# Optimization experiments

Hardware: AMD Instinct MI355X
Metric: run time of the kernel (lower is better)

The kernel has to match this reference:

```python
import jax, jax.numpy as jnp
import numpy as np

N_NODES = 100000
N_EDGES = 1600000
IN_FEATS, N_HIDDEN, N_CLASSES = 128, 64, 40


def setup_inputs() -> dict:
    key = jax.random.key(0)
    ks = jax.random.split(key, 6)
    h = jax.random.normal(ks[0], (N_NODES, IN_FEATS), dtype=jnp.float32)
    W0 = jax.random.normal(ks[1], (IN_FEATS, N_HIDDEN), dtype=jnp.float32) * (1.0 / np.sqrt(IN_FEATS))
    b0 = jnp.zeros((N_HIDDEN,), dtype=jnp.float32)
    W1 = jax.random.normal(ks[2], (N_HIDDEN, N_HIDDEN), dtype=jnp.float32) * (1.0 / np.sqrt(N_HIDDEN))
    b1 = jnp.zeros((N_HIDDEN,), dtype=jnp.float32)
    W2 = jax.random.normal(ks[3], (N_HIDDEN, N_CLASSES), dtype=jnp.float32) * (1.0 / np.sqrt(N_HIDDEN))
    b2 = jnp.zeros((N_CLASSES,), dtype=jnp.float32)
    src = jax.random.randint(ks[4], (N_EDGES,), 0, N_NODES, dtype=jnp.int32)
    dst = jax.random.randint(ks[5], (N_EDGES,), 0, N_NODES, dtype=jnp.int32)
    return {"h": h, "W0": W0, "b0": b0, "W1": W1, "b1": b1, "W2": W2, "b2": b2, "src": src, "dst": dst}


def _degrees(src, dst):
    ones = jnp.ones(src.shape[0], dtype=jnp.float32)
    out_deg = jax.ops.segment_sum(ones, src, num_segments=N_NODES)
    in_deg = jax.ops.segment_sum(ones, dst, num_segments=N_NODES)
    # DGL clamps degrees to >= 1 (allow_zero_in_degree)
    norm_src = jax.lax.rsqrt(jnp.maximum(out_deg, 1.0))  # [N]
    norm_dst = jax.lax.rsqrt(jnp.maximum(in_deg, 1.0))   # [N]
    return norm_src, norm_dst


def _graph_conv(x, W, b, src, dst, norm_src, norm_dst, act):
    # DGL GraphConv, norm='both': D_in^{-1/2} A^T D_out^{-1/2} (X W) + b
    xw = (x @ W) * norm_src[:, None]               # [N, out]
    agg = jax.ops.segment_sum(xw[src], dst, num_segments=N_NODES)  # gather-scatter over edges
    out = agg * norm_dst[:, None] + b
    return jax.nn.relu(out) if act else out


def reference(h, W0, b0, W1, b1, W2, b2, src, dst):
    norm_src, norm_dst = _degrees(src, dst)
    h = _graph_conv(h, W0, b0, src, dst, norm_src, norm_dst, act=True)
    # dropout layers are identity at inference
    h = _graph_conv(h, W1, b1, src, dst, norm_src, norm_dst, act=True)
    h = _graph_conv(h, W2, b2, src, dst, norm_src, norm_dst, act=False)
    return h
```

## Files before the change

kernel.cpp:

```cpp
#include <hip/hip_runtime.h>
#include <hip/hip_fp16.h>

#define N_NODES 100000
#define N_EDGES 1600000
#define ELL_W 64
#define NCHUNK 64
#define NSEG 4
#define CH (N_EDGES / NCHUNK)
#define SEGN (N_NODES / NSEG)

typedef _Float16 half8 __attribute__((ext_vector_type(8)));
typedef float floatx4 __attribute__((ext_vector_type(4)));


__global__ __launch_bounds__(512) void k_count(const int* __restrict__ src, const int* __restrict__ dst,
                                               unsigned char* __restrict__ cnt_out,
                                               unsigned char* __restrict__ cnt_in) {
    __shared__ unsigned pk[SEGN];
    const int c = blockIdx.x;
    const int lo = blockIdx.y * SEGN;
    for (int i = threadIdx.x; i < SEGN; i += 512) pk[i] = 0;
    __syncthreads();
    const int4* s4 = (const int4*)(src + c * CH);
    const int4* d4 = (const int4*)(dst + c * CH);
    for (int i = threadIdx.x; i < CH / 4; i += 512) {
        int4 s = s4[i], d = d4[i];
        unsigned a;
        a = (unsigned)(s.x - lo); if (a < SEGN) atomicAdd(&pk[a], 0x10000u);
        a = (unsigned)(s.y - lo); if (a < SEGN) atomicAdd(&pk[a], 0x10000u);
        a = (unsigned)(s.z - lo); if (a < SEGN) atomicAdd(&pk[a], 0x10000u);
        a = (unsigned)(s.w - lo); if (a < SEGN) atomicAdd(&pk[a], 0x10000u);
        a = (unsigned)(d.x - lo); if (a < SEGN) atomicAdd(&pk[a], 1u);
        a = (unsigned)(d.y - lo); if (a < SEGN) atomicAdd(&pk[a], 1u);
        a = (unsigned)(d.z - lo); if (a < SEGN) atomicAdd(&pk[a], 1u);
        a = (unsigned)(d.w - lo); if (a < SEGN) atomicAdd(&pk[a], 1u);
    }
    __syncthreads();
    for (int i = threadIdx.x; i < SEGN; i += 512) {
        unsigned v = pk[i];
        cnt_in [c * N_NODES + lo + i] = (unsigned char)(v & 0xFFFF);
        cnt_out[c * N_NODES + lo + i] = (unsigned char)(v >> 16);
    }
}

__global__ __launch_bounds__(256) void k_scan(unsigned char* __restrict__ cnt_in,
                                              const unsigned char* __restrict__ cnt_out,
                                              int* __restrict__ fill, float* __restrict__ norm_src,
                                              float* __restrict__ norm_dst) {
    int d = blockIdx.x * 256 + threadIdx.x;
    if (d >= N_NODES) return;
    int run = 0;
    for (int c = 0; c < NCHUNK; ++c) {
        int v = cnt_in[c * N_NODES + d];
        cnt_in[c * N_NODES + d] = (unsigned char)run;
        run += v;
    }
    int od = 0;
    for (int c = 0; c < NCHUNK; ++c) od += cnt_out[c * N_NODES + d];
    fill[d] = run;
    norm_dst[d] = rsqrtf((float)(run < 1 ? 1 : run));
    norm_src[d] = rsqrtf((float)(od  < 1 ? 1 : od ));
}

__global__ __launch_bounds__(512) void k_scatter(const int* __restrict__ src, const int* __restrict__ dst,
                                                 const unsigned char* __restrict__ bases,
                                                 int* __restrict__ ell) {
    __shared__ unsigned base[SEGN / 2];
    const int c = blockIdx.x;
    const int lo = blockIdx.y * SEGN;
    for (int i = threadIdx.x; i < SEGN / 2; i += 512) {
        unsigned b0 = bases[c * N_NODES + lo + 2 * i];
        unsigned b1 = bases[c * N_NODES + lo + 2 * i + 1];
        base[i] = b0 | (b1 << 16);
    }
    __syncthreads();
    const int4* s4 = (const int4*)(src + c * CH);
    const int4* d4 = (const int4*)(dst + c * CH);
    for (int i = threadIdx.x; i < CH / 4; i += 512) {
        int4 s = s4[i], d = d4[i];
        unsigned r, sh, old; int p;
        r = (unsigned)(d.x - lo); if (r < SEGN) { sh = (r & 1) << 4; old = atomicAdd(&base[r >> 1], 1u << sh); p = (old >> sh) & 0xFFFF; if (p < ELL_W) ell[p * N_NODES + lo + r] = s.x; }
        r = (unsigned)(d.y - lo); if (r < SEGN) { sh = (r & 1) << 4; old = atomicAdd(&base[r >> 1], 1u << sh); p = (old >> sh) & 0xFFFF; if (p < ELL_W) ell[p * N_NODES + lo + r] = s.y; }
        r = (unsigned)(d.z - lo); if (r < SEGN) { sh = (r & 1) << 4; old = atomicAdd(&base[r >> 1], 1u << sh); p = (old >> sh) & 0xFFFF; if (p < ELL_W) ell[p * N_NODES + lo + r] = s.z; }
        r = (unsigned)(d.w - lo); if (r < SEGN) { sh = (r & 1) << 4; old = atomicAdd(&base[r >> 1], 1u << sh); p = (old >> sh) & 0xFFFF; if (p < ELL_W) ell[p * N_NODES + lo + r] = s.w; }
    }
}

__device__ __forceinline__ void acc16B(const float4& v, float* acc) {
    const __half2* hh = (const __half2*)&v;
    #pragma unroll
    for (int t = 0; t < 4; ++t) {
        float2 f = __half22float2(hh[t]);
        acc[2 * t + 0] += f.x;
        acc[2 * t + 1] += f.y;
    }
}

template<int K, int NCOL>
__global__ __launch_bounds__(256) void k_gemm(const float* __restrict__ Xv, const float* __restrict__ W,
                                              const float* __restrict__ norm, __half* __restrict__ Y) {
    constexpr int NT = (NCOL + 15) / 16;
    constexpr int NR = NT * 16;
    __shared__ __align__(16) _Float16 Xh[64][K + 8];
    __shared__ __align__(16) _Float16 Wt[NR][K + 8];
    const int tid = threadIdx.x;
    const int row0 = blockIdx.x * 64;

    for (int idx = tid; idx < K * NCOL; idx += 256) {
        int k = idx / NCOL, c = idx - (idx / NCOL) * NCOL;
        Wt[c][k] = (_Float16)W[idx];
    }
    for (int idx = tid; idx < (NR - NCOL) * K; idx += 256) {
        int c = NCOL + idx / K, k = idx - (idx / K) * K;
        Wt[c][k] = (_Float16)0;
    }

    for (int idx = tid; idx < 64 * (K / 8); idx += 256) {
        int r = idx / (K / 8), kc = idx - (idx / (K / 8)) * (K / 8);
        int gr = row0 + r;
        half8 v = {0, 0, 0, 0, 0, 0, 0, 0};
        if (gr < N_NODES) {
            const float* X = Xv + (long)gr * K + kc * 8;
            float4 u0 = *(const float4*)(X + 0);
            float4 u1 = *(const float4*)(X + 4);
            v.s0 = (_Float16)u0.x; v.s1 = (_Float16)u0.y;
            v.s2 = (_Float16)u0.z; v.s3 = (_Float16)u0.w;
            v.s4 = (_Float16)u1.x; v.s5 = (_Float16)u1.y;
            v.s6 = (_Float16)u1.z; v.s7 = (_Float16)u1.w;
        }
        *(half8*)&Xh[r][kc * 8] = v;
    }
    __syncthreads();

    const int lane = tid & 63;
    const int wave = tid >> 6;
    const int quad = lane >> 4;
    const int l16 = lane & 15;
    const int r0 = wave * 16;

    floatx4 acc[NT] = {};
    #pragma unroll
    for (int k0 = 0; k0 < K; k0 += 32) {
        half8 a = *(const half8*)&Xh[r0 + l16][k0 + quad * 8];
        #pragma unroll
        for (int t = 0; t < NT; ++t) {
            half8 b = *(const half8*)&Wt[t * 16 + l16][k0 + quad * 8];
            acc[t] = __builtin_amdgcn_mfma_f32_16x16x32_f16(a, b, acc[t], 0, 0, 0);
        }
    }

    #pragma unroll
    for (int i = 0; i < 4; ++i) {
        int gr = row0 + r0 + quad * 4 + i;
        if (gr < N_NODES) {
            float s = norm[gr];
            #pragma unroll
            for (int t = 0; t < NT; ++t) {
                int c = t * 16 + l16;
                if (c < NCOL) Y[(long)gr * NCOL + c] = __float2half(acc[t][i] * s);
            }
        }
    }
}

template<int K, int NCOL>
__global__ __launch_bounds__(256) void k_agg_gemm(const __half* __restrict__ XWp, const int* __restrict__ ell,
                                                  const int* __restrict__ deg, const float* __restrict__ norm_dst,
                                                  const float* __restrict__ biasp, const float* __restrict__ W,
                                                  const float* __restrict__ norm, __half* __restrict__ Y) {
    constexpr int NT = (NCOL + 15) / 16;
    constexpr int NR = NT * 16;
    constexpr int NQ = K / 8;
    __shared__ __align__(16) _Float16 Xh[64][K + 8];
    __shared__ __align__(16) _Float16 Wt[NR][K + 8];
    __shared__ int sIdx[64][65];
    __shared__ int sDeg[64];
    __shared__ int sMax;
    const int tid = threadIdx.x;
    const int row0 = blockIdx.x * 64;

    for (int idx = tid; idx < K * NCOL; idx += 256) {
        int k = idx / NCOL, c = idx - (idx / NCOL) * NCOL;
        Wt[c][k] = (_Float16)W[idx];
    }
    for (int idx = tid; idx < (NR - NCOL) * K; idx += 256) {
        int c = NCOL + idx / K, k = idx - (idx / K) * K;
        Wt[c][k] = (_Float16)0;
    }

    if (tid < 64) {
        int node = row0 + tid;
        int dg = 0;
        if (node < N_NODES) { dg = deg[node]; if (dg > ELL_W) dg = ELL_W; }
        sDeg[tid] = dg;
        int v = dg;
        #pragma unroll
        for (int o = 32; o > 0; o >>= 1) v = max(v, __shfl_down(v, o));
        if (tid == 0) sMax = v;
    }
    __syncthreads();
    const int mdeg = sMax;
    for (int i = tid; i < mdeg * 64; i += 256) {
        int slot = i >> 6, r = i & 63;
        int node = row0 + r;
        sIdx[r][slot] = (node < N_NODES) ? ell[slot * N_NODES + node] : 0;
    }
    __syncthreads();

    for (int item = tid; item < 64 * NQ; item += 256) {
        int r = item / NQ, q = item - (item / NQ) * NQ;
        int d = row0 + r;
        int dg = sDeg[r];
        const int* idxr = sIdx[r];
        float acc[8] = {};
        int j = 0;
        for (; j + 8 <= dg; j += 8) {
            float4 v[8];
            #pragma unroll
            for (int u = 0; u < 8; ++u)
                v[u] = *(const float4*)(XWp + (long)idxr[j + u] * K + q * 8);
            #pragma unroll
            for (int u = 0; u < 8; ++u) acc16B(v[u], acc);
        }
        for (; j < dg; ++j) {
            float4 rv = *(const float4*)(XWp + (long)idxr[j] * K + q * 8);
            acc16B(rv, acc);
        }
        _Float16 res[8] = {};
        if (d < N_NODES) {
            float nd = norm_dst[d];
            #pragma unroll
            for (int t = 0; t < 8; ++t) {
                float o = acc[t] * nd + biasp[q * 8 + t];
                res[t] = (_Float16)fmaxf(o, 0.f);
            }
        }
        *(half8*)&Xh[r][q * 8] = *(const half8*)res;
    }
    __syncthreads();

    const int lane = tid & 63;
    const int wave = tid >> 6;
    const int quad = lane >> 4;
    const int l16 = lane & 15;
    const int r0 = wave * 16;

    floatx4 acc[NT] = {};
    #pragma unroll
    for (int k0 = 0; k0 < K; k0 += 32) {
        half8 a = *(const half8*)&Xh[r0 + l16][k0 + quad * 8];
        #pragma unroll
        for (int t = 0; t < NT; ++t) {
            half8 b = *(const half8*)&Wt[t * 16 + l16][k0 + quad * 8];
            acc[t] = __builtin_amdgcn_mfma_f32_16x16x32_f16(a, b, acc[t], 0, 0, 0);
        }
    }

    #pragma unroll
    for (int i = 0; i < 4; ++i) {
        int gr = row0 + r0 + quad * 4 + i;
        if (gr < N_NODES) {
            float s = norm[gr];
            #pragma unroll
            for (int t = 0; t < NT; ++t) {
                int c = t * 16 + l16;
                if (c < NCOL) Y[(long)gr * NCOL + c] = __float2half(acc[t][i] * s);
            }
        }
    }
}

template<int NF>
__global__ __launch_bounds__(320) void k_agg_f(const __half* __restrict__ XW, const int* __restrict__ ell,
                                               const int* __restrict__ deg, const float* __restrict__ norm_dst,
                                               const float* __restrict__ bias, float* __restrict__ OUT) {
    constexpr int NQ = NF / 8;
    __shared__ int sIdx[64][65];
    __shared__ int sDeg[64];
    __shared__ int sMax;
    const int tid = threadIdx.x;
    const int row0 = blockIdx.x * 64;

    if (tid < 64) {
        int node = row0 + tid;
        int dg = 0;
        if (node < N_NODES) { dg = deg[node]; if (dg > ELL_W) dg = ELL_W; }
        sDeg[tid] = dg;
        int v = dg;
        #pragma unroll
        for (int o = 32; o > 0; o >>= 1) v = max(v, __shfl_down(v, o));
        if (tid == 0) sMax = v;
    }
    __syncthreads();
    const int mdeg = sMax;
    for (int i = tid; i < mdeg * 64; i += 320) {
        int slot = i >> 6, r = i & 63;
        int node = row0 + r;
        sIdx[r][slot] = (node < N_NODES) ? ell[slot * N_NODES + node] : 0;
    }
    __syncthreads();

    const int r = tid / NQ, q = tid - (tid / NQ) * NQ;
    const int d = row0 + r;
    if (d >= N_NODES) return;
    const int dg = sDeg[r];
    const int* idxr = sIdx[r];

    float acc[8] = {};
    int j = 0;
    for (; j + 8 <= dg; j += 8) {
        float4 v[8];
        #pragma unroll
        for (int u = 0; u < 8; ++u)
            v[u] = *(const float4*)(XW + (long)idxr[j + u] * NF + q * 8);
        #pragma unroll
        for (int u = 0; u < 8; ++u) acc16B(v[u], acc);
    }
    for (; j < dg; ++j) {
        float4 rv = *(const float4*)(XW + (long)idxr[j] * NF + q * 8);
        acc16B(rv, acc);
    }

    float nd = norm_dst[d];
    float o[8];
    #pragma unroll
    for (int t = 0; t < 8; ++t) o[t] = acc[t] * nd + bias[q * 8 + t];
    *(float4*)(OUT + (long)d * NF + q * 8 + 0) = make_float4(o[0], o[1], o[2], o[3]);
    *(float4*)(OUT + (long)d * NF + q * 8 + 4) = make_float4(o[4], o[5], o[6], o[7]);
}

extern "C" void kernel_launch(void* const* d_in, const int* in_sizes, int n_in,
                              void* d_out, int out_size, void* d_ws, size_t ws_size,
                              hipStream_t stream) {
    const float* h  = (const float*)d_in[0];
    const float* W0 = (const float*)d_in[1];
    const float* b0 = (const float*)d_in[2];
    const float* W1 = (const float*)d_in[3];
    const float* b1 = (const float*)d_in[4];
    const float* W2 = (const float*)d_in[5];
    const float* b2 = (const float*)d_in[6];
    const int* src  = (const int*)d_in[7];
    const int* dst  = (const int*)d_in[8];
    float* out = (float*)d_out;

    char* ws = (char*)d_ws;
    size_t off = 0;
    int* fill        = (int*)(ws + off); off += (size_t)N_NODES * 4;
    float* norm_src  = (float*)(ws + off); off += (size_t)N_NODES * 4;
    float* norm_dst  = (float*)(ws + off); off += (size_t)N_NODES * 4;
    int* ell         = (int*)(ws + off); off += (size_t)N_NODES * ELL_W * 4;
    unsigned char* cnt_in  = (unsigned char*)(ws + off); off += (size_t)NCHUNK * N_NODES;
    unsigned char* cnt_out = (unsigned char*)(ws + off); off += (size_t)NCHUNK * N_NODES;
    __half* bufA  = (__half*)(ws + off); off += (size_t)N_NODES * 64 * 2;
    __half* bufB  = (__half*)(ws + off); off += (size_t)N_NODES * 64 * 2;

    k_count<<<dim3(NCHUNK, NSEG), 512, 0, stream>>>(src, dst, cnt_out, cnt_in);
    k_scan<<<(N_NODES + 255) / 256, 256, 0, stream>>>(cnt_in, cnt_out, fill, norm_src, norm_dst);
    k_scatter<<<dim3(NCHUNK, NSEG), 512, 0, stream>>>(src, dst, cnt_in, ell);

    const int grid = (N_NODES + 63) / 64;

    k_gemm<128, 64><<<grid, 256, 0, stream>>>(h, W0, norm_src, bufA);
    k_agg_gemm<64, 64><<<grid, 256, 0, stream>>>(bufA, ell, fill, norm_dst, b0, W1, norm_src, bufB);
    k_agg_gemm<64, 40><<<grid, 256, 0, stream>>>(bufB, ell, fill, norm_dst, b1, W2, norm_src, bufA);
    k_agg_f<40><<<grid, 320, 0, stream>>>(bufA, ell, fill, norm_dst, b2, out);
}
```

Measured before the change: 274.3 us.

## Store ELL neighbor lists row-major and read indices directly in aggregation

Changes the ELL adjacency layout from slot-major to node-major (64 contiguous ints per node), so each destination's neighbor list is contiguous. The aggregation kernels drop the shared-memory index staging, two barriers and the max-degree reduction, and instead read indices with int4 vector loads straight from global memory, with an unrolled tail. Scatter writes become scattered across rows rather than coalesced per slot, and several threads of the same row now reload the same index lines, relying on the cache.

```diff
diff --git a/kernel.cpp b/kernel.cpp
--- a/kernel.cpp
+++ b/kernel.cpp
@@ -79,10 +79,10 @@
     for (int i = threadIdx.x; i < CH / 4; i += 512) {
         int4 s = s4[i], d = d4[i];
         unsigned r, sh, old; int p;
-        r = (unsigned)(d.x - lo); if (r < SEGN) { sh = (r & 1) << 4; old = atomicAdd(&base[r >> 1], 1u << sh); p = (old >> sh) & 0xFFFF; if (p < ELL_W) ell[p * N_NODES + lo + r] = s.x; }
-        r = (unsigned)(d.y - lo); if (r < SEGN) { sh = (r & 1) << 4; old = atomicAdd(&base[r >> 1], 1u << sh); p = (old >> sh) & 0xFFFF; if (p < ELL_W) ell[p * N_NODES + lo + r] = s.y; }
-        r = (unsigned)(d.z - lo); if (r < SEGN) { sh = (r & 1) << 4; old = atomicAdd(&base[r >> 1], 1u << sh); p = (old >> sh) & 0xFFFF; if (p < ELL_W) ell[p * N_NODES + lo + r] = s.z; }
-        r = (unsigned)(d.w - lo); if (r < SEGN) { sh = (r & 1) << 4; old = atomicAdd(&base[r >> 1], 1u << sh); p = (old >> sh) & 0xFFFF; if (p < ELL_W) ell[p * N_NODES + lo + r] = s.w; }
+        r = (unsigned)(d.x - lo); if (r < SEGN) { sh = (r & 1) << 4; old = atomicAdd(&base[r >> 1], 1u << sh); p = (old >> sh) & 0xFFFF; if (p < ELL_W) ell[(((long)(lo + r)) << 6) + p] = s.x; }
+        r = (unsigned)(d.y - lo); if (r < SEGN) { sh = (r & 1) << 4; old = atomicAdd(&base[r >> 1], 1u << sh); p = (old >> sh) & 0xFFFF; if (p < ELL_W) ell[(((long)(lo + r)) << 6) + p] = s.y; }
+        r = (unsigned)(d.z - lo); if (r < SEGN) { sh = (r & 1) << 4; old = atomicAdd(&base[r >> 1], 1u << sh); p = (old >> sh) & 0xFFFF; if (p < ELL_W) ell[(((long)(lo + r)) << 6) + p] = s.z; }
+        r = (unsigned)(d.w - lo); if (r < SEGN) { sh = (r & 1) << 4; old = atomicAdd(&base[r >> 1], 1u << sh); p = (old >> sh) & 0xFFFF; if (p < ELL_W) ell[(((long)(lo + r)) << 6) + p] = s.w; }
     }
 }
 
@@ -173,9 +173,6 @@
     constexpr int NQ = K / 8;
     __shared__ __align__(16) _Float16 Xh[64][K + 8];
     __shared__ __align__(16) _Float16 Wt[NR][K + 8];
-    __shared__ int sIdx[64][65];
-    __shared__ int sDeg[64];
-    __shared__ int sMax;
     const int tid = threadIdx.x;
     const int row0 = blockIdx.x * 64;
 
@@ -188,46 +185,41 @@
         Wt[c][k] = (_Float16)0;
     }
 
-    if (tid < 64) {
-        int node = row0 + tid;
-        int dg = 0;
-        if (node < N_NODES) { dg = deg[node]; if (dg > ELL_W) dg = ELL_W; }
-        sDeg[tid] = dg;
-        int v = dg;
-        #pragma unroll
-        for (int o = 32; o > 0; o >>= 1) v = max(v, __shfl_down(v, o));
-        if (tid == 0) sMax = v;
-    }
-    __syncthreads();
-    const int mdeg = sMax;
-    for (int i = tid; i < mdeg * 64; i += 256) {
-        int slot = i >> 6, r = i & 63;
-        int node = row0 + r;
-        sIdx[r][slot] = (node < N_NODES) ? ell[slot * N_NODES + node] : 0;
-    }
-    __syncthreads();
-
     for (int item = tid; item < 64 * NQ; item += 256) {
         int r = item / NQ, q = item - (item / NQ) * NQ;
         int d = row0 + r;
-        int dg = sDeg[r];
-        const int* idxr = sIdx[r];
-        float acc[8] = {};
-        int j = 0;
-        for (; j + 8 <= dg; j += 8) {
-            float4 v[8];
-            #pragma unroll
-            for (int u = 0; u < 8; ++u)
-                v[u] = *(const float4*)(XWp + (long)idxr[j + u] * K + q * 8);
-            #pragma unroll
-            for (int u = 0; u < 8; ++u) acc16B(v[u], acc);
-        }
-        for (; j < dg; ++j) {
-            float4 rv = *(const float4*)(XWp + (long)idxr[j] * K + q * 8);
-            acc16B(rv, acc);
-        }
         _Float16 res[8] = {};
         if (d < N_NODES) {
+            int dg = deg[d]; if (dg > ELL_W) dg = ELL_W;
+            const int* idxr = ell + (((long)d) << 6);
+            float acc[8] = {};
+            for (int j = 0; j < dg; j += 8) {
+                int4 i0 = *(const int4*)(idxr + j);
+                int4 i1 = *(const int4*)(idxr + j + 4);
+                int id0 = i0.x, id1 = i0.y, id2 = i0.z, id3 = i0.w;
+                int id4 = i1.x, id5 = i1.y, id6 = i1.z, id7 = i1.w;
+                if (j + 8 <= dg) {
+                    float4 v0 = *(const float4*)(XWp + (long)id0 * K + q * 8);
+                    float4 v1 = *(const float4*)(XWp + (long)id1 * K + q * 8);
+                    float4 v2 = *(const float4*)(XWp + (long)id2 * K + q * 8);
+                    float4 v3 = *(const float4*)(XWp + (long)id3 * K + q * 8);
+                    float4 v4 = *(const float4*)(XWp + (long)id4 * K + q * 8);
+                    float4 v5 = *(const float4*)(XWp + (long)id5 * K + q * 8);
+                    float4 v6 = *(const float4*)(XWp + (long)id6 * K + q * 8);
+                    float4 v7 = *(const float4*)(XWp + (long)id7 * K + q * 8);
+                    acc16B(v0, acc); acc16B(v1, acc); acc16B(v2, acc); acc16B(v3, acc);
+                    acc16B(v4, acc); acc16B(v5, acc); acc16B(v6, acc); acc16B(v7, acc);
+                } else {
+                    int rem = dg - j;
+                    if (0 < rem) { float4 v = *(const float4*)(XWp + (long)id0 * K + q * 8); acc16B(v, acc); }
+                    if (1 < rem) { float4 v = *(const float4*)(XWp + (long)id1 * K + q * 8); acc16B(v, acc); }
+                    if (2 < rem) { float4 v = *(const float4*)(XWp + (long)id2 * K + q * 8); acc16B(v, acc); }
+                    if (3 < rem) { float4 v = *(const float4*)(XWp + (long)id3 * K + q * 8); acc16B(v, acc); }
+                    if (4 < rem) { float4 v = *(const float4*)(XWp + (long)id4 * K + q * 8); acc16B(v, acc); }
+                    if (5 < rem) { float4 v = *(const float4*)(XWp + (long)id5 * K + q * 8); acc16B(v, acc); }
+                    if (6 < rem) { float4 v = *(const float4*)(XWp + (long)id6 * K + q * 8); acc16B(v, acc); }
+                }
+            }
             float nd = norm_dst[d];
             #pragma unroll
             for (int t = 0; t < 8; ++t) {
@@ -275,50 +267,42 @@
                                                const int* __restrict__ deg, const float* __restrict__ norm_dst,
                                                const float* __restrict__ bias, float* __restrict__ OUT) {
     constexpr int NQ = NF / 8;
-    __shared__ int sIdx[64][65];
-    __shared__ int sDeg[64];
-    __shared__ int sMax;
     const int tid = threadIdx.x;
     const int row0 = blockIdx.x * 64;
-
-    if (tid < 64) {
-        int node = row0 + tid;
-        int dg = 0;
-        if (node < N_NODES) { dg = deg[node]; if (dg > ELL_W) dg = ELL_W; }
-        sDeg[tid] = dg;
-        int v = dg;
-        #pragma unroll
-        for (int o = 32; o > 0; o >>= 1) v = max(v, __shfl_down(v, o));
-        if (tid == 0) sMax = v;
-    }
-    __syncthreads();
-    const int mdeg = sMax;
-    for (int i = tid; i < mdeg * 64; i += 320) {
-        int slot = i >> 6, r = i & 63;
-        int node = row0 + r;
-        sIdx[r][slot] = (node < N_NODES) ? ell[slot * N_NODES + node] : 0;
-    }
-    __syncthreads();
 
     const int r = tid / NQ, q = tid - (tid / NQ) * NQ;
     const int d = row0 + r;
     if (d >= N_NODES) return;
-    const int dg = sDeg[r];
-    const int* idxr = sIdx[r];
+    int dg = deg[d]; if (dg > ELL_W) dg = ELL_W;
+    const int* idxr = ell + (((long)d) << 6);
 
     float acc[8] = {};
-    int j = 0;
-    for (; j + 8 <= dg; j += 8) {
-        float4 v[8];
-        #pragma unroll
-        for (int u = 0; u < 8; ++u)
-            v[u] = *(const float4*)(XW + (long)idxr[j + u] * NF + q * 8);
-        #pragma unroll
-        for (int u = 0; u < 8; ++u) acc16B(v[u], acc);
-    }
-    for (; j < dg; ++j) {
-        float4 rv = *(const float4*)(XW + (long)idxr[j] * NF + q * 8);
-        acc16B(rv, acc);
+    for (int j = 0; j < dg; j += 8) {
+        int4 i0 = *(const int4*)(idxr + j);
+        int4 i1 = *(const int4*)(idxr + j + 4);
+        int id0 = i0.x, id1 = i0.y, id2 = i0.z, id3 = i0.w;
+        int id4 = i1.x, id5 = i1.y, id6 = i1.z, id7 = i1.w;
+        if (j + 8 <= dg) {
+            float4 v0 = *(const float4*)(XW + (long)id0 * NF + q * 8);
+            float4 v1 = *(const float4*)(XW + (long)id1 * NF + q * 8);
+            float4 v2 = *(const float4*)(XW + (long)id2 * NF + q * 8);
+            float4 v3 = *(const float4*)(XW + (long)id3 * NF + q * 8);
+            float4 v4 = *(const float4*)(XW + (long)id4 * NF + q * 8);
+            float4 v5 = *(const float4*)(XW + (long)id5 * NF + q * 8);
+            float4 v6 = *(const float4*)(XW + (long)id6 * NF + q * 8);
+            float4 v7 = *(const float4*)(XW + (long)id7 * NF + q * 8);
+            acc16B(v0, acc); acc16B(v1, acc); acc16B(v2, acc); acc16B(v3, acc);
+            acc16B(v4, acc); acc16B(v5, acc); acc16B(v6, acc); acc16B(v7, acc);
+        } else {
+            int rem = dg - j;
+            if (0 < rem) { float4 v = *(const float4*)(XW + (long)id0 * NF + q * 8); acc16B(v, acc); }
+            if (1 < rem) { float4 v = *(const float4*)(XW + (long)id1 * NF + q * 8); acc16B(v, acc); }
+            if (2 < rem) { float4 v = *(const float4*)(XW + (long)id2 * NF + q * 8); acc16B(v, acc); }
+            if (3 < rem) { float4 v = *(const float4*)(XW + (long)id3 * NF + q * 8); acc16B(v, acc); }
+            if (4 < rem) { float4 v = *(const float4*)(XW + (long)id4 * NF + q * 8); acc16B(v, acc); }
+            if (5 < rem) { float4 v = *(const float4*)(XW + (long)id5 * NF + q * 8); acc16B(v, acc); }
+            if (6 < rem) { float4 v = *(const float4*)(XW + (long)id6 * NF + q * 8); acc16B(v, acc); }
+        }
     }
 
     float nd = norm_dst[d];
```

Result: slower. 296.8 us (+8.2%).
